# Optimization experiments

Hardware: AMD Instinct MI355X
Metric: run time of the kernel (lower is better)

## Reference

```python
import jax, jax.numpy as jnp
import numpy as np
import math

N, E = 1000, 128000
IN_DIM, HID, OUT_DIM = 256, 512, 16
L, H = 6, 8
C = HID // H  # 64, TransformerConv out_channels per head
EDGE_DIM = 32
MAX_LEN = 1000


def _pe(max_len, d_model):
    pos = np.arange(max_len)[:, None].astype(np.float32)
    div = np.exp(np.arange(0, d_model, 2).astype(np.float32) * (-math.log(10000.0) / d_model))
    pe = np.zeros((max_len, d_model), dtype=np.float32)
    pe[:, 0::2] = np.sin(pos * div)
    pe[:, 1::2] = np.cos(pos * div)
    return jnp.asarray(pe)


def setup_inputs() -> dict:
    key = jax.random.key(0)
    ks = jax.random.split(key, 32)
    g = lambda k, shape, fan_in: jax.random.normal(k, shape, jnp.float32) / jnp.sqrt(jnp.float32(fan_in))
    inp = {
        "x": jax.random.normal(ks[0], (N, IN_DIM), jnp.float32),
        "edge_index": jax.random.randint(ks[1], (2, E), 0, N, jnp.int64 if jax.config.jax_enable_x64 else jnp.int32),
        "edge_attr": jax.random.uniform(ks[2], (E, 4), jnp.float32),
        "embed_w": g(ks[3], (IN_DIM, HID), IN_DIM),
        "embed_b": jnp.zeros((HID,), jnp.float32),
        "pe": _pe(MAX_LEN, HID),
        "ee_w1": g(ks[4], (4, 16), 4), "ee_b1": jnp.zeros((16,), jnp.float32),
        "ee_w2": g(ks[5], (16, EDGE_DIM), 16), "ee_b2": jnp.zeros((EDGE_DIM,), jnp.float32),
        "q_w": g(ks[6], (L, HID, HID), HID), "q_b": jnp.zeros((L, HID), jnp.float32),
        "k_w": g(ks[7], (L, HID, HID), HID), "k_b": jnp.zeros((L, HID), jnp.float32),
        "v_w": g(ks[8], (L, HID, HID), HID), "v_b": jnp.zeros((L, HID), jnp.float32),
        "e_w": g(ks[9], (L, EDGE_DIM, HID), EDGE_DIM),
        "skip_w": g(ks[10], (L, HID, HID), HID), "skip_b": jnp.zeros((L, HID), jnp.float32),
        "ln_g": jnp.ones((L, HID), jnp.float32), "ln_b": jnp.zeros((L, HID), jnp.float32),
        "dom_w": g(ks[11], (HID, 16), HID), "dom_b": jnp.zeros((16,), jnp.float32),
        "cls_w1": g(ks[12], (HID + 16, HID // 2), HID + 16), "cls_b1": jnp.zeros((HID // 2,), jnp.float32),
        "cls_w2": g(ks[13], (HID // 2, OUT_DIM), HID // 2), "cls_b2": jnp.zeros((OUT_DIM,), jnp.float32),
    }
    return inp


def _layer_norm(x, g, b, eps=1e-5):
    mu = jnp.mean(x, axis=-1, keepdims=True)
    var = jnp.var(x, axis=-1, keepdims=True)
    return (x - mu) * jax.lax.rsqrt(var + eps) * g + b


def _forward(x, edge_index, edge_attr, embed_w, embed_b, pe, ee_w1, ee_b1, ee_w2, ee_b2,
             q_w, q_b, k_w, k_b, v_w, v_b, e_w, skip_w, skip_b, ln_g, ln_b,
             dom_w, dom_b, cls_w1, cls_b1, cls_w2, cls_b2):
    n = x.shape[0]
    h = x @ embed_w + embed_b
    h = h + pe[:n]
    # edge encoder: 4 -> 16 -> 32
    ef = jax.nn.relu(edge_attr @ ee_w1 + ee_b1) @ ee_w2 + ee_b2  # [E, 32]
    src, tgt = edge_index[0], edge_index[1]
    scale = 1.0 / math.sqrt(C)
    for l in range(L):
        res = h
        q = (h @ q_w[l] + q_b[l]).reshape(n, H, C)
        k = (h @ k_w[l] + k_b[l]).reshape(n, H, C)
        v = (h @ v_w[l] + v_b[l]).reshape(n, H, C)
        e = (ef @ e_w[l]).reshape(-1, H, C)            # [E, H, C], lin_edge has no bias
        kj = k[src] + e                                 # gather + edge bias
        score = jnp.sum(q[tgt] * kj, axis=-1) * scale   # [E, H]
        # segment softmax over incoming edges of each target node
        m = jax.ops.segment_max(score, tgt, num_segments=n)     # [N, H]
        al = jnp.exp(score - m[tgt])
        den = jax.ops.segment_sum(al, tgt, num_segments=n)      # [N, H]
        al = al / den[tgt]
        msg = (v[src] + e) * al[:, :, None]             # [E, H, C]
        out = jax.ops.segment_sum(msg, tgt, num_segments=n).reshape(n, HID)
        out = out + h @ skip_w[l] + skip_b[l]           # root_weight skip
        h = _layer_norm(out + res, ln_g[l], ln_b[l])
    dom = h @ dom_w + dom_b                             # [N, 16]
    comb = jnp.concatenate([h, dom], axis=-1)
    hid = jax.nn.relu(comb @ cls_w1 + cls_b1)
    return hid @ cls_w2 + cls_b2


def reference(x, edge_index, edge_attr, embed_w, embed_b, pe, ee_w1, ee_b1, ee_w2, ee_b2,
              q_w, q_b, k_w, k_b, v_w, v_b, e_w, skip_w, skip_b, ln_g, ln_b,
              dom_w, dom_b, cls_w1, cls_b1, cls_w2, cls_b2):
    return _forward(x, edge_index, edge_attr, embed_w, embed_b, pe, ee_w1, ee_b1, ee_w2, ee_b2,
                    q_w, q_b, k_w, k_b, v_w, v_b, e_w, skip_w, skip_b, ln_g, ln_b,
                    dom_w, dom_b, cls_w1, cls_b1, cls_w2, cls_b2)
```

## Files before the change

kernel.cpp:

```cpp
#include <hip/hip_runtime.h>
#include <hip/hip_bf16.h>
#include <cstdint>
#include <cstddef>

#define NN 1000
#define EE 128000
#define LAYERS 6
#define SCALE 0.125f
#define MAXDEG 320

typedef __attribute__((ext_vector_type(4))) float f32x4;
typedef __attribute__((ext_vector_type(8))) short short8v;

static __device__ __forceinline__ unsigned short f2bf(float x){
    unsigned int u = __float_as_uint(x);
    unsigned int lsb = (u >> 16) & 1u;
    u += 0x7fffu + lsb;
    return (unsigned short)(u >> 16);
}
static __device__ __forceinline__ float bf2f(unsigned short u){
    return __uint_as_float(((unsigned int)u) << 16);
}

__global__ void zero_counts(int* cnt){
    cnt[threadIdx.x] = 0;
}

__global__ void hist_kernel(const int* __restrict__ tgt, int* cnt){
    int e = blockIdx.x*256 + threadIdx.x;
    if (e < EE) atomicAdd(&cnt[tgt[e]], 1);
}

__global__ void scan_kernel(const int* __restrict__ cnt, int* offs, int* cursor){
    __shared__ int s[1024];
    int tid = threadIdx.x;
    s[tid] = (tid < NN) ? cnt[tid] : 0;
    __syncthreads();
    for (int st = 1; st < 1024; st <<= 1){
        int v = (tid >= st) ? s[tid-st] : 0;
        __syncthreads();
        s[tid] += v;
        __syncthreads();
    }
    int excl = (tid == 0) ? 0 : s[tid-1];
    if (tid < NN){ offs[tid] = excl; cursor[tid] = excl; }
    if (tid == 0) offs[NN] = s[NN-1];
}

__global__ void scatter_kernel(const int* __restrict__ src, const int* __restrict__ tgt,
                               int* cursor, int* ssrc, int* epos){
    int e = blockIdx.x*256 + threadIdx.x;
    if (e < EE){
        int t = tgt[e];
        int pos = atomicAdd(&cursor[t], 1);
        ssrc[pos] = src[e];
        epos[e] = pos;
    }
}

__global__ __launch_bounds__(256) void edge_enc(
    const float* __restrict__ edge_attr,
    const float* __restrict__ w1, const float* __restrict__ b1,
    const float* __restrict__ w2, const float* __restrict__ b2,
    const int* __restrict__ epos,
    unsigned short* __restrict__ efs)
{
    __shared__ float w1s[64], b1s[16], w2s[512], b2s[32];
    int tid = threadIdx.x;
    if (tid < 64) w1s[tid] = w1[tid];
    if (tid < 16) b1s[tid] = b1[tid];
    if (tid < 32) b2s[tid] = b2[tid];
    w2s[tid] = w2[tid];
    w2s[tid+256] = w2[tid+256];
    __syncthreads();
    int e = blockIdx.x*256 + tid;
    if (e >= EE) return;
    float4 av = *(const float4*)(edge_attr + (size_t)e*4);
    float hd[16];
    #pragma unroll
    for (int i = 0; i < 16; i++){
        float v = av.x*w1s[i] + av.y*w1s[16+i] + av.z*w1s[32+i] + av.w*w1s[48+i] + b1s[i];
        hd[i] = fmaxf(v, 0.f);
    }
    unsigned short* op = efs + (size_t)epos[e]*32;
    #pragma unroll
    for (int k4 = 0; k4 < 8; k4++){
        ushort4 ub;
        float v0 = b2s[k4*4+0], v1 = b2s[k4*4+1], v2 = b2s[k4*4+2], v3 = b2s[k4*4+3];
        #pragma unroll
        for (int i = 0; i < 16; i++){
            float hv = hd[i];
            v0 += hv*w2s[i*32 + k4*4+0];
            v1 += hv*w2s[i*32 + k4*4+1];
            v2 += hv*w2s[i*32 + k4*4+2];
            v3 += hv*w2s[i*32 + k4*4+3];
        }
        ub.x = f2bf(v0); ub.y = f2bf(v1); ub.z = f2bf(v2); ub.w = f2bf(v3);
        *(ushort4*)(op + k4*4) = ub;
    }
}

__global__ __launch_bounds__(256) void convert_all(
    const float* __restrict__ Wq, const float* __restrict__ Wk,
    const float* __restrict__ Wv, const float* __restrict__ Ws,
    const float* __restrict__ embed_w, const float* __restrict__ x,
    unsigned short* __restrict__ Wt, unsigned short* __restrict__ ewt,
    unsigned short* __restrict__ xb)
{
    int bid = blockIdx.x;
    int tid = threadIdx.x;
    if (bid < 6144){
        int mm = bid >> 8;
        int tile = bid & 255;
        int tk = tile >> 4, tn = tile & 15;
        int l = mm >> 2, m = mm & 3;
        const float* W = ((m==0)?Wq:(m==1)?Wk:(m==2)?Wv:Ws) + (size_t)l*512*512;
        unsigned short* dst = Wt + (size_t)mm*512*512;
        __shared__ float ts[32][33];
        int r = tid >> 3, c0 = (tid & 7)*4;
        float4 v = *(const float4*)(W + (size_t)(tk*32 + r)*512 + tn*32 + c0);
        ts[r][c0+0] = v.x; ts[r][c0+1] = v.y; ts[r][c0+2] = v.z; ts[r][c0+3] = v.w;
        __syncthreads();
        ushort4 o;
        o.x = f2bf(ts[c0+0][r]); o.y = f2bf(ts[c0+1][r]);
        o.z = f2bf(ts[c0+2][r]); o.w = f2bf(ts[c0+3][r]);
        *(ushort4*)(dst + (size_t)(tn*32 + r)*512 + tk*32 + c0) = o;
    } else if (bid < 6144 + 128){
        int tile = bid - 6144;
        int tn = tile & 15, tk = tile >> 4;
        __shared__ float ts2[32][33];
        int r = tid >> 3, c0 = (tid & 7)*4;
        float4 v = *(const float4*)(embed_w + (size_t)(tk*32 + r)*512 + tn*32 + c0);
        ts2[r][c0+0] = v.x; ts2[r][c0+1] = v.y; ts2[r][c0+2] = v.z; ts2[r][c0+3] = v.w;
        __syncthreads();
        ushort4 o;
        o.x = f2bf(ts2[c0+0][r]); o.y = f2bf(ts2[c0+1][r]);
        o.z = f2bf(ts2[c0+2][r]); o.w = f2bf(ts2[c0+3][r]);
        *(ushort4*)(ewt + (size_t)(tn*32 + r)*256 + tk*32 + c0) = o;
    } else {
        int row = bid - 6144 - 128;
        xb[(size_t)row*256 + tid] = (row < NN) ? f2bf(x[(size_t)row*256 + tid]) : (unsigned short)0;
    }
}

__global__ __launch_bounds__(256) void gemm_embed_mfma(
    const unsigned short* __restrict__ xb,
    const unsigned short* __restrict__ ewt,
    const float* __restrict__ bias, const float* __restrict__ pe,
    float* __restrict__ C, unsigned short* __restrict__ hb)
{
    int bid = blockIdx.x;
    int mt = bid >> 2, nt = bid & 3;
    int row0 = mt*64, col0 = nt*128;

    __shared__ __align__(16) unsigned short As[64*40];
    __shared__ __align__(16) unsigned short Bs[128*40];

    int tid = threadIdx.x;
    int wid = tid >> 6, l = tid & 63;
    int wm = wid >> 1, wn = wid & 1;

    f32x4 acc[2][4] = {};
    int ar = tid >> 2, akq = tid & 3;
    for (int k0 = 0; k0 < 256; k0 += 32){
        *(uint4*)&As[ar*40 + akq*8]      = *(const uint4*)&xb[(size_t)(row0+ar)*256 + k0 + akq*8];
        *(uint4*)&Bs[ar*40 + akq*8]      = *(const uint4*)&ewt[(size_t)(col0+ar)*256 + k0 + akq*8];
        *(uint4*)&Bs[(ar+64)*40 + akq*8] = *(const uint4*)&ewt[(size_t)(col0+ar+64)*256 + k0 + akq*8];
        __syncthreads();
        short8v a0 = *(const short8v*)&As[(wm*32 + (l&15))*40 + (l>>4)*8];
        short8v a1 = *(const short8v*)&As[(wm*32 + 16 + (l&15))*40 + (l>>4)*8];
        #pragma unroll
        for (int nj = 0; nj < 4; nj++){
            short8v b = *(const short8v*)&Bs[(wn*64 + nj*16 + (l&15))*40 + (l>>4)*8];
            acc[0][nj] = __builtin_amdgcn_mfma_f32_16x16x32_bf16(a0, b, acc[0][nj], 0, 0, 0);
            acc[1][nj] = __builtin_amdgcn_mfma_f32_16x16x32_bf16(a1, b, acc[1][nj], 0, 0, 0);
        }
        __syncthreads();
    }
    int rbase = (l >> 4)*4, cl = l & 15;
    #pragma unroll
    for (int mi = 0; mi < 2; mi++)
        #pragma unroll
        for (int nj = 0; nj < 4; nj++)
            #pragma unroll
            for (int r = 0; r < 4; r++){
                int grow = row0 + wm*32 + mi*16 + rbase + r;
                int gcol = col0 + wn*64 + nj*16 + cl;
                if (grow < NN){
                    float v = acc[mi][nj][r] + bias[gcol] + pe[(size_t)grow*512 + gcol];
                    C[(size_t)grow*512 + gcol] = v;
                    hb[(size_t)grow*512 + gcol] = f2bf(v);
                }
            }
}

__global__ __launch_bounds__(256) void gemm_qkvs_mfma(
    const unsigned short* __restrict__ hb,
    const unsigned short* __restrict__ Wt,
    const float* __restrict__ qb, const float* __restrict__ kb,
    const float* __restrict__ vb, const float* __restrict__ sb,
    float* __restrict__ Q, unsigned short* __restrict__ K16,
    unsigned short* __restrict__ V16, float* __restrict__ S)
{
    int bid = blockIdx.x;
    int mat = bid >> 7;
    int rem = bid & 127;
    int mt = rem >> 3, nt = rem & 7;
    int row0 = mt*64, col0 = nt*64;
    const unsigned short* W = Wt + (size_t)mat*512*512;
    const float* bias = (mat==0)?qb:(mat==1)?kb:(mat==2)?vb:sb;

    __shared__ __align__(16) unsigned short As[64*72];
    __shared__ __align__(16) unsigned short Bs[64*72];

    int tid = threadIdx.x;
    int wid = tid >> 6, l = tid & 63;
    int wm = wid >> 1, wn = wid & 1;

    f32x4 acc[2][2] = {};
    int lr = tid >> 2;
    int lc = (tid & 3)*2;
    const unsigned short* ga = hb + (size_t)(row0+lr)*512 + lc*8;
    const unsigned short* gb = W  + (size_t)(col0+lr)*512 + lc*8;

    uint4 ra0 = *(const uint4*)(ga);
    uint4 ra1 = *(const uint4*)(ga + 8);
    uint4 rb0 = *(const uint4*)(gb);
    uint4 rb1 = *(const uint4*)(gb + 8);

    for (int k0 = 0; k0 < 512; k0 += 64){
        __syncthreads();
        *(uint4*)&As[lr*72 + lc*8]     = ra0;
        *(uint4*)&As[lr*72 + lc*8 + 8] = ra1;
        *(uint4*)&Bs[lr*72 + lc*8]     = rb0;
        *(uint4*)&Bs[lr*72 + lc*8 + 8] = rb1;
        __syncthreads();
        if (k0 + 64 < 512){
            ra0 = *(const uint4*)(ga + k0 + 64);
            ra1 = *(const uint4*)(ga + k0 + 72);
            rb0 = *(const uint4*)(gb + k0 + 64);
            rb1 = *(const uint4*)(gb + k0 + 72);
        }
        #pragma unroll
        for (int ks = 0; ks < 2; ks++){
            short8v a0 = *(const short8v*)&As[(wm*32 + (l&15))*72      + ks*32 + (l>>4)*8];
            short8v a1 = *(const short8v*)&As[(wm*32 + 16 + (l&15))*72 + ks*32 + (l>>4)*8];
            short8v b0 = *(const short8v*)&Bs[(wn*32 + (l&15))*72      + ks*32 + (l>>4)*8];
            short8v b1 = *(const short8v*)&Bs[(wn*32 + 16 + (l&15))*72 + ks*32 + (l>>4)*8];
            acc[0][0] = __builtin_amdgcn_mfma_f32_16x16x32_bf16(a0, b0, acc[0][0], 0, 0, 0);
            acc[0][1] = __builtin_amdgcn_mfma_f32_16x16x32_bf16(a0, b1, acc[0][1], 0, 0, 0);
            acc[1][0] = __builtin_amdgcn_mfma_f32_16x16x32_bf16(a1, b0, acc[1][0], 0, 0, 0);
            acc[1][1] = __builtin_amdgcn_mfma_f32_16x16x32_bf16(a1, b1, acc[1][1], 0, 0, 0);
        }
    }
    int rbase = (l >> 4)*4, cl = l & 15;
    #pragma unroll
    for (int mi = 0; mi < 2; mi++)
        #pragma unroll
        for (int nj = 0; nj < 2; nj++)
            #pragma unroll
            for (int r = 0; r < 4; r++){
                int grow = row0 + wm*32 + mi*16 + rbase + r;
                int gcol = col0 + wn*32 + nj*16 + cl;
                if (grow < NN){
                    float v = acc[mi][nj][r] + bias[gcol];
                    if (mat == 0)      Q[(size_t)grow*512 + gcol] = v;
                    else if (mat == 1) K16[(size_t)grow*512 + gcol] = f2bf(v);
                    else if (mat == 2) V16[(size_t)grow*512 + gcol] = f2bf(v);
                    else               S[(size_t)grow*512 + gcol] = v;
                }
            }
}

__global__ __launch_bounds__(256) void attn_mfma(
    const float* __restrict__ Qm, const unsigned short* __restrict__ Km,
    const unsigned short* __restrict__ Vm,
    const unsigned short* __restrict__ efs, const float* __restrict__ e_w_l,
    const int* __restrict__ ssrc, const int* __restrict__ offs,
    float* __restrict__ x_pre)
{
    int tid = threadIdx.x;
    int t = blockIdx.x;

    __shared__ float q_s[512];
    __shared__ float qe_s[8*33];
    __shared__ __align__(16) unsigned short qb_s[512];
    __shared__ __align__(16) unsigned short qef_s[64*8];
    __shared__ float sc_s[MAXDEG*8];
    __shared__ int   src_s[MAXDEG];
    __shared__ float pv_s[2][512];
    __shared__ float pe_s[2][256];
    __shared__ float s_s[256];
    __shared__ float redm[32], redd[32];
    __shared__ float m_s[8], d_s[8];

    {
        float v0 = Qm[(size_t)t*512 + tid];
        float v1 = Qm[(size_t)t*512 + 256 + tid];
        q_s[tid] = v0; q_s[256+tid] = v1;
        qb_s[tid] = f2bf(v0); qb_s[256+tid] = f2bf(v1);
    }
    __syncthreads();
    {
        int hh = tid >> 5, dd = tid & 31;
        const float* wrow = e_w_l + (size_t)dd*512 + hh*64;
        const float* qh = q_s + hh*64;
        float a = 0.f;
        #pragma unroll
        for (int c = 0; c < 64; c++) a += qh[c]*wrow[c];
        qe_s[hh*33 + dd] = a;
    }
    __syncthreads();
    for (int idx = tid; idx < 512; idx += 256){
        int l = idx >> 3, j = idx & 7;
        int col = l & 15, d = (l >> 4)*8 + j;
        float v = (col < 8) ? qe_s[col*33 + d] : 0.f;
        qef_s[l*8 + j] = f2bf(v);
    }
    int start = offs[t], deg = offs[t+1] - start;
    __syncthreads();

    {
        int wv = tid >> 6, l = tid & 63;
        int arow = l & 15;
        int achk = (l >> 4)*8;
        const short8v bz = {0,0,0,0,0,0,0,0};
        for (int eg = wv*16; eg < deg; eg += 64){
            int e = eg + arow;
            int ec = (e < deg) ? e : 0;
            int s = ssrc[start + ec];
            if (achk == 0 && e < deg) src_s[e] = s;
            const unsigned short* kr = Km + (size_t)s*512 + achk;
            f32x4 acc = {0.f, 0.f, 0.f, 0.f};
            #pragma unroll
            for (int ks = 0; ks < 16; ks++){
                short8v a = *(const short8v*)(kr + ks*32);
                short8v b = (arow == (ks >> 1)) ? *(const short8v*)(qb_s + ks*32 + achk) : bz;
                acc = __builtin_amdgcn_mfma_f32_16x16x32_bf16(a, b, acc, 0, 0, 0);
            }
            {
                short8v a = *(const short8v*)(efs + (size_t)(start+ec)*32 + achk);
                short8v b = *(const short8v*)(qef_s + l*8);
                acc = __builtin_amdgcn_mfma_f32_16x16x32_bf16(a, b, acc, 0, 0, 0);
            }
            #pragma unroll
            for (int r = 0; r < 4; r++){
                int er = eg + (l >> 4)*4 + r;
                if (arow < 8 && er < deg) sc_s[er*8 + arow] = acc[r]*SCALE;
            }
        }
    }
    __syncthreads();

    {
        int he = tid & 7, ib = tid >> 3;
        float lm = -1e30f;
        for (int i = ib; i < deg; i += 32) lm = fmaxf(lm, sc_s[i*8 + he]);
        lm = fmaxf(lm, __shfl_xor(lm, 8));
        lm = fmaxf(lm, __shfl_xor(lm, 16));
        lm = fmaxf(lm, __shfl_xor(lm, 32));
        if ((tid & 63) < 8) redm[(tid>>6)*8 + (tid & 7)] = lm;
    }
    __syncthreads();
    if (tid < 8) m_s[tid] = fmaxf(fmaxf(redm[tid], redm[8+tid]), fmaxf(redm[16+tid], redm[24+tid]));
    __syncthreads();

    {
        int he = tid & 7, ib = tid >> 3;
        float mh = m_s[he];
        float den = 0.f;
        for (int i = ib; i < deg; i += 32){
            float al = __expf(sc_s[i*8 + he] - mh);
            sc_s[i*8 + he] = al;
            den += al;
        }
        den += __shfl_xor(den, 8);
        den += __shfl_xor(den, 16);
        den += __shfl_xor(den, 32);
        if ((tid & 63) < 8) redd[(tid>>6)*8 + (tid & 7)] = den;
    }
    __syncthreads();
    if (tid < 8) d_s[tid] = redd[tid] + redd[8+tid] + redd[16+tid] + redd[24+tid];
    __syncthreads();

    {
        int g = tid >> 7, q7 = tid & 127;
        int c4 = q7*4;
        int h2 = c4 >> 6;
        int hE = q7 >> 4, dE = (q7 & 15)*2;
        float4 accV = make_float4(0.f, 0.f, 0.f, 0.f);
        float2 accE = make_float2(0.f, 0.f);
        #pragma unroll 2
        for (int i = g; i < deg; i += 2){
            int s = src_s[i];
            float al = sc_s[i*8 + h2];
            float alE = sc_s[i*8 + hE];
            ushort4 v = *(const ushort4*)(Vm + (size_t)s*512 + c4);
            unsigned int e2 = *(const unsigned int*)(efs + (size_t)(start+i)*32 + dE);
            accV.x += al*bf2f(v.x); accV.y += al*bf2f(v.y);
            accV.z += al*bf2f(v.z); accV.w += al*bf2f(v.w);
            accE.x += alE*bf2f((unsigned short)(e2 & 0xffffu));
            accE.y += alE*bf2f((unsigned short)(e2 >> 16));
        }
        *(float4*)&pv_s[g][c4] = accV;
        *(float2*)&pe_s[g][hE*32 + dE] = accE;
    }
    __syncthreads();
    {
        float dv = d_s[tid >> 5];
        float invd = (dv > 0.f) ? 1.f/dv : 0.f;
        s_s[tid] = (pe_s[0][tid] + pe_s[1][tid]) * invd;
    }
    __syncthreads();

    {
        int c0 = tid, c1 = tid + 256;
        int h0 = c0 >> 6, h1 = c1 >> 6;
        float dv0 = d_s[h0], dv1 = d_s[h1];
        float i0 = (dv0 > 0.f) ? 1.f/dv0 : 0.f;
        float i1 = (dv1 > 0.f) ? 1.f/dv1 : 0.f;
        float r0 = (pv_s[0][c0] + pv_s[1][c0]) * i0;
        float r1 = (pv_s[0][c1] + pv_s[1][c1]) * i1;
        float oe0 = 0.f, oe1 = 0.f;
        const float* sp0 = s_s + h0*32;
        const float* sp1 = s_s + h1*32;
        #pragma unroll
        for (int d = 0; d < 32; d++){
            oe0 += sp0[d]*e_w_l[(size_t)d*512 + c0];
            oe1 += sp1[d]*e_w_l[(size_t)d*512 + c1];
        }
        x_pre[(size_t)t*512 + c0] = r0 + oe0;
        x_pre[(size_t)t*512 + c1] = r1 + oe1;
    }
}

__global__ __launch_bounds__(256) void ln_skip(
    const float* __restrict__ x_pre, const float* __restrict__ SKm,
    const float* __restrict__ hcur,
    const float* __restrict__ ln_g_l, const float* __restrict__ ln_b_l,
    float* __restrict__ hnext, unsigned short* __restrict__ hbn)
{
    int tid = threadIdx.x, t = blockIdx.x;
    __shared__ float red[4], red2[4];
    float x0 = x_pre[(size_t)t*512 + tid]       + SKm[(size_t)t*512 + tid]       + hcur[(size_t)t*512 + tid];
    float x1 = x_pre[(size_t)t*512 + 256 + tid] + SKm[(size_t)t*512 + 256 + tid] + hcur[(size_t)t*512 + 256 + tid];
    float sA = x0 + x1, sB = x0*x0 + x1*x1;
    #pragma unroll
    for (int m = 1; m <= 32; m <<= 1){
        sA += __shfl_xor(sA, m);
        sB += __shfl_xor(sB, m);
    }
    int wv = tid >> 6, ln = tid & 63;
    if (ln == 0){ red[wv] = sA; red2[wv] = sB; }
    __syncthreads();
    float tot  = red[0] + red[1] + red[2] + red[3];
    float tot2 = red2[0] + red2[1] + red2[2] + red2[3];
    float mu  = tot*(1.f/512.f);
    float var = tot2*(1.f/512.f) - mu*mu;
    float rstd = rsqrtf(var + 1e-5f);
    float y0 = (x0 - mu)*rstd*ln_g_l[tid]     + ln_b_l[tid];
    float y1 = (x1 - mu)*rstd*ln_g_l[256+tid] + ln_b_l[256+tid];
    hnext[(size_t)t*512 + tid]       = y0;
    hnext[(size_t)t*512 + 256 + tid] = y1;
    hbn[(size_t)t*512 + tid]       = f2bf(y0);
    hbn[(size_t)t*512 + 256 + tid] = f2bf(y1);
}

__global__ __launch_bounds__(256) void final_head(
    const float* __restrict__ hin,
    const float* __restrict__ dom_w, const float* __restrict__ dom_b,
    const float* __restrict__ w1, const float* __restrict__ b1,
    const float* __restrict__ w2, const float* __restrict__ b2,
    float* __restrict__ out)
{
    int tid = threadIdx.x, t = blockIdx.x;
    __shared__ float h_s[512];
    __shared__ float dom_s[16];
    __shared__ float hid_s[256];
    __shared__ float red[256];
    h_s[tid]     = hin[(size_t)t*512 + tid];
    h_s[tid+256] = hin[(size_t)t*512 + 256 + tid];
    __syncthreads();
    if (tid < 16){
        float a = dom_b[tid];
        for (int i = 0; i < 512; i++) a += h_s[i]*dom_w[i*16 + tid];
        dom_s[tid] = a;
    }
    __syncthreads();
    float acc = b1[tid];
    for (int i = 0; i < 512; i++) acc += h_s[i]*w1[(size_t)i*256 + tid];
    #pragma unroll
    for (int i = 0; i < 16; i++) acc += dom_s[i]*w1[(size_t)(512+i)*256 + tid];
    hid_s[tid] = fmaxf(acc, 0.f);
    __syncthreads();
    int o = tid & 15, g = tid >> 4;
    float p = 0.f;
    #pragma unroll
    for (int j = 0; j < 16; j++) p += hid_s[g*16 + j]*w2[(g*16 + j)*16 + o];
    red[tid] = p;
    __syncthreads();
    if (tid < 16){
        float s2 = b2[tid];
        for (int gg = 0; gg < 16; gg++) s2 += red[gg*16 + tid];
        out[(size_t)t*16 + tid] = s2;
    }
}

extern "C" void kernel_launch(void* const* d_in, const int* in_sizes, int n_in,
                              void* d_out, int out_size, void* d_ws, size_t ws_size,
                              hipStream_t stream)
{
    const float* x       = (const float*)d_in[0];
    const int*   eidx    = (const int*)  d_in[1];
    const float* eattr   = (const float*)d_in[2];
    const float* embed_w = (const float*)d_in[3];
    const float* embed_b = (const float*)d_in[4];
    const float* pe      = (const float*)d_in[5];
    const float* ee_w1   = (const float*)d_in[6];
    const float* ee_b1   = (const float*)d_in[7];
    const float* ee_w2   = (const float*)d_in[8];
    const float* ee_b2   = (const float*)d_in[9];
    const float* q_w     = (const float*)d_in[10];
    const float* q_b     = (const float*)d_in[11];
    const float* k_w     = (const float*)d_in[12];
    const float* k_b     = (const float*)d_in[13];
    const float* v_w     = (const float*)d_in[14];
    const float* v_b     = (const float*)d_in[15];
    const float* e_w     = (const float*)d_in[16];
    const float* skip_w  = (const float*)d_in[17];
    const float* skip_b  = (const float*)d_in[18];
    const float* ln_g    = (const float*)d_in[19];
    const float* ln_b    = (const float*)d_in[20];
    const float* dom_w   = (const float*)d_in[21];
    const float* dom_b   = (const float*)d_in[22];
    const float* cls_w1  = (const float*)d_in[23];
    const float* cls_b1  = (const float*)d_in[24];
    const float* cls_w2  = (const float*)d_in[25];
    const float* cls_b2  = (const float*)d_in[26];
    float* out = (float*)d_out;

    float* ws = (float*)d_ws;
    size_t o = 0;
    float* h0    = ws + o; o += (size_t)512*NN;
    float* h1    = ws + o; o += (size_t)512*NN;
    float* Qb    = ws + o; o += (size_t)512*NN;
    float* Sb    = ws + o; o += (size_t)512*NN;
    float* xpre  = ws + o; o += (size_t)512*NN;
    unsigned short* Kb16 = (unsigned short*)(ws + o); o += (size_t)1024*512/2;
    unsigned short* Vb16 = (unsigned short*)(ws + o); o += (size_t)1024*512/2;
    unsigned short* efs  = (unsigned short*)(ws + o); o += (size_t)EE*32/2;
    unsigned short* hb   = (unsigned short*)(ws + o); o += (size_t)1024*512/2;
    unsigned short* xb   = (unsigned short*)(ws + o); o += (size_t)1024*256/2;
    unsigned short* ewt  = (unsigned short*)(ws + o); o += (size_t)512*256/2;
    unsigned short* Wtb  = (unsigned short*)(ws + o); o += (size_t)24*512*512/2;
    int* cnt    = (int*)(ws + o); o += 1024;
    int* offs   = (int*)(ws + o); o += 1024;
    int* cursor = (int*)(ws + o); o += 1024;
    int* ssrc   = (int*)(ws + o); o += EE;
    int* epos   = (int*)(ws + o); o += EE;

    const int* srcp = eidx;
    const int* tgtp = eidx + EE;

    zero_counts<<<1, 1024, 0, stream>>>(cnt);
    hist_kernel<<<EE/256, 256, 0, stream>>>(tgtp, cnt);
    scan_kernel<<<1, 1024, 0, stream>>>(cnt, offs, cursor);
    scatter_kernel<<<EE/256, 256, 0, stream>>>(srcp, tgtp, cursor, ssrc, epos);
    edge_enc<<<EE/256, 256, 0, stream>>>(eattr, ee_w1, ee_b1, ee_w2, ee_b2, epos, efs);
    convert_all<<<6144 + 128 + 1024, 256, 0, stream>>>(q_w, k_w, v_w, skip_w, embed_w, x, Wtb, ewt, xb);
    gemm_embed_mfma<<<64, 256, 0, stream>>>(xb, ewt, embed_b, pe, h0, hb);

    float* hc = h0;
    float* hn = h1;
    for (int l = 0; l < LAYERS; l++){
        gemm_qkvs_mfma<<<512, 256, 0, stream>>>(
            hb, Wtb + (size_t)l*4*512*512,
            q_b + (size_t)l*512, k_b + (size_t)l*512,
            v_b + (size_t)l*512, skip_b + (size_t)l*512,
            Qb, Kb16, Vb16, Sb);
        attn_mfma<<<NN, 256, 0, stream>>>(
            Qb, Kb16, Vb16, efs, e_w + (size_t)l*32*512,
            ssrc, offs, xpre);
        ln_skip<<<NN, 256, 0, stream>>>(
            xpre, Sb, hc,
            ln_g + (size_t)l*512, ln_b + (size_t)l*512,
            hn, hb);
        float* tmp = hc; hc = hn; hn = tmp;
    }
    final_head<<<NN, 256, 0, stream>>>(hc, dom_w, dom_b, cls_w1, cls_b1, cls_w2, cls_b2, out);
}
```

Measured before the change: 581.8 us.

## Double-buffer QKVS GEMM, fuse LayerNorm into attention, drop softmax max pass

```diff
diff --git a/kernel.cpp b/kernel.cpp
--- a/kernel.cpp
+++ b/kernel.cpp
@@ -210,8 +210,8 @@
     const unsigned short* W = Wt + (size_t)mat*512*512;
     const float* bias = (mat==0)?qb:(mat==1)?kb:(mat==2)?vb:sb;
 
-    __shared__ __align__(16) unsigned short As[64*72];
-    __shared__ __align__(16) unsigned short Bs[64*72];
+    __shared__ __align__(16) unsigned short As[2][64*72];
+    __shared__ __align__(16) unsigned short Bs[2][64*72];
 
     int tid = threadIdx.x;
     int wid = tid >> 6, l = tid & 63;
@@ -227,32 +227,50 @@
     uint4 ra1 = *(const uint4*)(ga + 8);
     uint4 rb0 = *(const uint4*)(gb);
     uint4 rb1 = *(const uint4*)(gb + 8);
-
-    for (int k0 = 0; k0 < 512; k0 += 64){
-        __syncthreads();
-        *(uint4*)&As[lr*72 + lc*8]     = ra0;
-        *(uint4*)&As[lr*72 + lc*8 + 8] = ra1;
-        *(uint4*)&Bs[lr*72 + lc*8]     = rb0;
-        *(uint4*)&Bs[lr*72 + lc*8 + 8] = rb1;
-        __syncthreads();
-        if (k0 + 64 < 512){
-            ra0 = *(const uint4*)(ga + k0 + 64);
-            ra1 = *(const uint4*)(ga + k0 + 72);
-            rb0 = *(const uint4*)(gb + k0 + 64);
-            rb1 = *(const uint4*)(gb + k0 + 72);
-        }
+    *(uint4*)&As[0][lr*72 + lc*8]     = ra0;
+    *(uint4*)&As[0][lr*72 + lc*8 + 8] = ra1;
+    *(uint4*)&Bs[0][lr*72 + lc*8]     = rb0;
+    *(uint4*)&Bs[0][lr*72 + lc*8 + 8] = rb1;
+    ra0 = *(const uint4*)(ga + 64);
+    ra1 = *(const uint4*)(ga + 72);
+    rb0 = *(const uint4*)(gb + 64);
+    rb1 = *(const uint4*)(gb + 72);
+    __syncthreads();
+
+    #pragma unroll
+    for (int t = 0; t < 8; t++){
+        int cur = t & 1;
+        short8v a0f[2], a1f[2], b0f[2], b1f[2];
         #pragma unroll
         for (int ks = 0; ks < 2; ks++){
-            short8v a0 = *(const short8v*)&As[(wm*32 + (l&15))*72      + ks*32 + (l>>4)*8];
-            short8v a1 = *(const short8v*)&As[(wm*32 + 16 + (l&15))*72 + ks*32 + (l>>4)*8];
-            short8v b0 = *(const short8v*)&Bs[(wn*32 + (l&15))*72      + ks*32 + (l>>4)*8];
-            short8v b1 = *(const short8v*)&Bs[(wn*32 + 16 + (l&15))*72 + ks*32 + (l>>4)*8];
-            acc[0][0] = __builtin_amdgcn_mfma_f32_16x16x32_bf16(a0, b0, acc[0][0], 0, 0, 0);
-            acc[0][1] = __builtin_amdgcn_mfma_f32_16x16x32_bf16(a0, b1, acc[0][1], 0, 0, 0);
-            acc[1][0] = __builtin_amdgcn_mfma_f32_16x16x32_bf16(a1, b0, acc[1][0], 0, 0, 0);
-            acc[1][1] = __builtin_amdgcn_mfma_f32_16x16x32_bf16(a1, b1, acc[1][1], 0, 0, 0);
-        }
-    }
+            a0f[ks] = *(const short8v*)&As[cur][(wm*32 + (l&15))*72      + ks*32 + (l>>4)*8];
+            a1f[ks] = *(const short8v*)&As[cur][(wm*32 + 16 + (l&15))*72 + ks*32 + (l>>4)*8];
+            b0f[ks] = *(const short8v*)&Bs[cur][(wn*32 + (l&15))*72      + ks*32 + (l>>4)*8];
+            b1f[ks] = *(const short8v*)&Bs[cur][(wn*32 + 16 + (l&15))*72 + ks*32 + (l>>4)*8];
+        }
+        if (t < 7){
+            *(uint4*)&As[cur^1][lr*72 + lc*8]     = ra0;
+            *(uint4*)&As[cur^1][lr*72 + lc*8 + 8] = ra1;
+            *(uint4*)&Bs[cur^1][lr*72 + lc*8]     = rb0;
+            *(uint4*)&Bs[cur^1][lr*72 + lc*8 + 8] = rb1;
+        }
+        if (t + 2 < 8){
+            int k2 = (t + 2)*64;
+            ra0 = *(const uint4*)(ga + k2);
+            ra1 = *(const uint4*)(ga + k2 + 8);
+            rb0 = *(const uint4*)(gb + k2);
+            rb1 = *(const uint4*)(gb + k2 + 8);
+        }
+        #pragma unroll
+        for (int ks = 0; ks < 2; ks++){
+            acc[0][0] = __builtin_amdgcn_mfma_f32_16x16x32_bf16(a0f[ks], b0f[ks], acc[0][0], 0, 0, 0);
+            acc[0][1] = __builtin_amdgcn_mfma_f32_16x16x32_bf16(a0f[ks], b1f[ks], acc[0][1], 0, 0, 0);
+            acc[1][0] = __builtin_amdgcn_mfma_f32_16x16x32_bf16(a1f[ks], b0f[ks], acc[1][0], 0, 0, 0);
+            acc[1][1] = __builtin_amdgcn_mfma_f32_16x16x32_bf16(a1f[ks], b1f[ks], acc[1][1], 0, 0, 0);
+        }
+        if (t < 7) __syncthreads();
+    }
+
     int rbase = (l >> 4)*4, cl = l & 15;
     #pragma unroll
     for (int mi = 0; mi < 2; mi++)
@@ -277,7 +295,9 @@
     const unsigned short* __restrict__ Vm,
     const unsigned short* __restrict__ efs, const float* __restrict__ e_w_l,
     const int* __restrict__ ssrc, const int* __restrict__ offs,
-    float* __restrict__ x_pre)
+    const float* __restrict__ SKm, const float* __restrict__ hcur,
+    const float* __restrict__ ln_g_l, const float* __restrict__ ln_b_l,
+    float* __restrict__ hnext, unsigned short* __restrict__ hbn)
 {
     int tid = threadIdx.x;
     int t = blockIdx.x;
@@ -285,14 +305,15 @@
     __shared__ float q_s[512];
     __shared__ float qe_s[8*33];
     __shared__ __align__(16) unsigned short qb_s[512];
-    __shared__ __align__(16) unsigned short qef_s[64*8];
+    __shared__ __align__(16) unsigned short qbd_s[16*64*8];
     __shared__ float sc_s[MAXDEG*8];
     __shared__ int   src_s[MAXDEG];
-    __shared__ float pv_s[2][512];
-    __shared__ float pe_s[2][256];
+    __shared__ float pv_s[4][512];
+    __shared__ float pe_s[4][256];
     __shared__ float s_s[256];
-    __shared__ float redm[32], redd[32];
-    __shared__ float m_s[8], d_s[8];
+    __shared__ float redd[32];
+    __shared__ float d_s[8];
+    __shared__ float lredA[4], lredB[4];
 
     {
         float v0 = Qm[(size_t)t*512 + tid];
@@ -310,12 +331,16 @@
         for (int c = 0; c < 64; c++) a += qh[c]*wrow[c];
         qe_s[hh*33 + dd] = a;
     }
-    __syncthreads();
-    for (int idx = tid; idx < 512; idx += 256){
-        int l = idx >> 3, j = idx & 7;
-        int col = l & 15, d = (l >> 4)*8 + j;
-        float v = (col < 8) ? qe_s[col*33 + d] : 0.f;
-        qef_s[l*8 + j] = f2bf(v);
+    {
+        const uint4 z4 = {0u,0u,0u,0u};
+        #pragma unroll
+        for (int it = 0; it < 4; it++){
+            int idx = tid + it*256;
+            int ks = idx >> 6, lq = idx & 63;
+            int col = lq & 15;
+            uint4 v = (col == (ks >> 1)) ? *(const uint4*)&qb_s[ks*32 + (lq>>4)*8] : z4;
+            *(uint4*)&qbd_s[idx*8] = v;
+        }
     }
     int start = offs[t], deg = offs[t+1] - start;
     __syncthreads();
@@ -323,30 +348,44 @@
     {
         int wv = tid >> 6, l = tid & 63;
         int arow = l & 15;
-        int achk = (l >> 4)*8;
-        const short8v bz = {0,0,0,0,0,0,0,0};
+        int achk8 = (l >> 4)*8;
+        short8v bef;
+        {
+            int col = l & 15;
+            #pragma unroll
+            for (int j = 0; j < 8; j++){
+                float v = (col < 8) ? qe_s[col*33 + achk8 + j] : 0.f;
+                bef[j] = (short)f2bf(v);
+            }
+        }
         for (int eg = wv*16; eg < deg; eg += 64){
             int e = eg + arow;
             int ec = (e < deg) ? e : 0;
             int s = ssrc[start + ec];
-            if (achk == 0 && e < deg) src_s[e] = s;
-            const unsigned short* kr = Km + (size_t)s*512 + achk;
-            f32x4 acc = {0.f, 0.f, 0.f, 0.f};
+            if (achk8 == 0 && e < deg) src_s[e] = s;
+            const unsigned short* kr = Km + (size_t)s*512 + achk8;
+            f32x4 accA = {0.f, 0.f, 0.f, 0.f};
+            f32x4 accB = {0.f, 0.f, 0.f, 0.f};
             #pragma unroll
-            for (int ks = 0; ks < 16; ks++){
+            for (int ks = 0; ks < 8; ks++){
                 short8v a = *(const short8v*)(kr + ks*32);
-                short8v b = (arow == (ks >> 1)) ? *(const short8v*)(qb_s + ks*32 + achk) : bz;
-                acc = __builtin_amdgcn_mfma_f32_16x16x32_bf16(a, b, acc, 0, 0, 0);
+                short8v b = *(const short8v*)&qbd_s[(ks*64 + l)*8];
+                accA = __builtin_amdgcn_mfma_f32_16x16x32_bf16(a, b, accA, 0, 0, 0);
+            }
+            #pragma unroll
+            for (int ks = 8; ks < 16; ks++){
+                short8v a = *(const short8v*)(kr + ks*32);
+                short8v b = *(const short8v*)&qbd_s[(ks*64 + l)*8];
+                accB = __builtin_amdgcn_mfma_f32_16x16x32_bf16(a, b, accB, 0, 0, 0);
             }
             {
-                short8v a = *(const short8v*)(efs + (size_t)(start+ec)*32 + achk);
-                short8v b = *(const short8v*)(qef_s + l*8);
-                acc = __builtin_amdgcn_mfma_f32_16x16x32_bf16(a, b, acc, 0, 0, 0);
+                short8v a = *(const short8v*)(efs + (size_t)(start+ec)*32 + achk8);
+                accA = __builtin_amdgcn_mfma_f32_16x16x32_bf16(a, bef, accA, 0, 0, 0);
             }
             #pragma unroll
             for (int r = 0; r < 4; r++){
                 int er = eg + (l >> 4)*4 + r;
-                if (arow < 8 && er < deg) sc_s[er*8 + arow] = acc[r]*SCALE;
+                if (arow < 8 && er < deg) sc_s[er*8 + arow] = (accA[r] + accB[r])*SCALE;
             }
         }
     }
@@ -354,23 +393,9 @@
 
     {
         int he = tid & 7, ib = tid >> 3;
-        float lm = -1e30f;
-        for (int i = ib; i < deg; i += 32) lm = fmaxf(lm, sc_s[i*8 + he]);
-        lm = fmaxf(lm, __shfl_xor(lm, 8));
-        lm = fmaxf(lm, __shfl_xor(lm, 16));
-        lm = fmaxf(lm, __shfl_xor(lm, 32));
-        if ((tid & 63) < 8) redm[(tid>>6)*8 + (tid & 7)] = lm;
-    }
-    __syncthreads();
-    if (tid < 8) m_s[tid] = fmaxf(fmaxf(redm[tid], redm[8+tid]), fmaxf(redm[16+tid], redm[24+tid]));
-    __syncthreads();
-
-    {
-        int he = tid & 7, ib = tid >> 3;
-        float mh = m_s[he];
         float den = 0.f;
         for (int i = ib; i < deg; i += 32){
-            float al = __expf(sc_s[i*8 + he] - mh);
+            float al = __expf(sc_s[i*8 + he]);
             sc_s[i*8 + he] = al;
             den += al;
         }
@@ -384,32 +409,32 @@
     __syncthreads();
 
     {
-        int g = tid >> 7, q7 = tid & 127;
-        int c4 = q7*4;
-        int h2 = c4 >> 6;
-        int hE = q7 >> 4, dE = (q7 & 15)*2;
-        float4 accV = make_float4(0.f, 0.f, 0.f, 0.f);
-        float2 accE = make_float2(0.f, 0.f);
-        #pragma unroll 2
-        for (int i = g; i < deg; i += 2){
+        int g = tid >> 6, q6 = tid & 63;
+        int c8 = q6*8;
+        int h2 = q6 >> 3;
+        int dE4 = (q6 & 7)*4;
+        float accV[8] = {};
+        float accE[4] = {};
+        #pragma unroll 4
+        for (int i = g; i < deg; i += 4){
             int s = src_s[i];
             float al = sc_s[i*8 + h2];
-            float alE = sc_s[i*8 + hE];
-            ushort4 v = *(const ushort4*)(Vm + (size_t)s*512 + c4);
-            unsigned int e2 = *(const unsigned int*)(efs + (size_t)(start+i)*32 + dE);
-            accV.x += al*bf2f(v.x); accV.y += al*bf2f(v.y);
-            accV.z += al*bf2f(v.z); accV.w += al*bf2f(v.w);
-            accE.x += alE*bf2f((unsigned short)(e2 & 0xffffu));
-            accE.y += alE*bf2f((unsigned short)(e2 >> 16));
-        }
-        *(float4*)&pv_s[g][c4] = accV;
-        *(float2*)&pe_s[g][hE*32 + dE] = accE;
+            short8v v = *(const short8v*)(Vm + (size_t)s*512 + c8);
+            ushort4 e4 = *(const ushort4*)(efs + (size_t)(start+i)*32 + dE4);
+            #pragma unroll
+            for (int j = 0; j < 8; j++) accV[j] += al*bf2f((unsigned short)v[j]);
+            accE[0] += al*bf2f(e4.x); accE[1] += al*bf2f(e4.y);
+            accE[2] += al*bf2f(e4.z); accE[3] += al*bf2f(e4.w);
+        }
+        #pragma unroll
+        for (int j = 0; j < 8; j++) pv_s[g][c8+j] = accV[j];
+        *(float4*)&pe_s[g][h2*32 + dE4] = make_float4(accE[0], accE[1], accE[2], accE[3]);
     }
     __syncthreads();
     {
         float dv = d_s[tid >> 5];
         float invd = (dv > 0.f) ? 1.f/dv : 0.f;
-        s_s[tid] = (pe_s[0][tid] + pe_s[1][tid]) * invd;
+        s_s[tid] = (pe_s[0][tid] + pe_s[1][tid] + pe_s[2][tid] + pe_s[3][tid]) * invd;
     }
     __syncthreads();
 
@@ -419,8 +444,8 @@
         float dv0 = d_s[h0], dv1 = d_s[h1];
         float i0 = (dv0 > 0.f) ? 1.f/dv0 : 0.f;
         float i1 = (dv1 > 0.f) ? 1.f/dv1 : 0.f;
-        float r0 = (pv_s[0][c0] + pv_s[1][c0]) * i0;
-        float r1 = (pv_s[0][c1] + pv_s[1][c1]) * i1;
+        float r0 = (pv_s[0][c0] + pv_s[1][c0] + pv_s[2][c0] + pv_s[3][c0]) * i0;
+        float r1 = (pv_s[0][c1] + pv_s[1][c1] + pv_s[2][c1] + pv_s[3][c1]) * i1;
         float oe0 = 0.f, oe1 = 0.f;
         const float* sp0 = s_s + h0*32;
         const float* sp1 = s_s + h1*32;
@@ -429,41 +454,30 @@
             oe0 += sp0[d]*e_w_l[(size_t)d*512 + c0];
             oe1 += sp1[d]*e_w_l[(size_t)d*512 + c1];
         }
-        x_pre[(size_t)t*512 + c0] = r0 + oe0;
-        x_pre[(size_t)t*512 + c1] = r1 + oe1;
-    }
-}
-
-__global__ __launch_bounds__(256) void ln_skip(
-    const float* __restrict__ x_pre, const float* __restrict__ SKm,
-    const float* __restrict__ hcur,
-    const float* __restrict__ ln_g_l, const float* __restrict__ ln_b_l,
-    float* __restrict__ hnext, unsigned short* __restrict__ hbn)
-{
-    int tid = threadIdx.x, t = blockIdx.x;
-    __shared__ float red[4], red2[4];
-    float x0 = x_pre[(size_t)t*512 + tid]       + SKm[(size_t)t*512 + tid]       + hcur[(size_t)t*512 + tid];
-    float x1 = x_pre[(size_t)t*512 + 256 + tid] + SKm[(size_t)t*512 + 256 + tid] + hcur[(size_t)t*512 + 256 + tid];
-    float sA = x0 + x1, sB = x0*x0 + x1*x1;
-    #pragma unroll
-    for (int m = 1; m <= 32; m <<= 1){
-        sA += __shfl_xor(sA, m);
-        sB += __shfl_xor(sB, m);
-    }
-    int wv = tid >> 6, ln = tid & 63;
-    if (ln == 0){ red[wv] = sA; red2[wv] = sB; }
-    __syncthreads();
-    float tot  = red[0] + red[1] + red[2] + red[3];
-    float tot2 = red2[0] + red2[1] + red2[2] + red2[3];
-    float mu  = tot*(1.f/512.f);
-    float var = tot2*(1.f/512.f) - mu*mu;
-    float rstd = rsqrtf(var + 1e-5f);
-    float y0 = (x0 - mu)*rstd*ln_g_l[tid]     + ln_b_l[tid];
-    float y1 = (x1 - mu)*rstd*ln_g_l[256+tid] + ln_b_l[256+tid];
-    hnext[(size_t)t*512 + tid]       = y0;
-    hnext[(size_t)t*512 + 256 + tid] = y1;
-    hbn[(size_t)t*512 + tid]       = f2bf(y0);
-    hbn[(size_t)t*512 + 256 + tid] = f2bf(y1);
+        float x0 = r0 + oe0 + SKm[(size_t)t*512 + c0] + hcur[(size_t)t*512 + c0];
+        float x1 = r1 + oe1 + SKm[(size_t)t*512 + c1] + hcur[(size_t)t*512 + c1];
+
+        float sA = x0 + x1, sB = x0*x0 + x1*x1;
+        #pragma unroll
+        for (int m2 = 1; m2 <= 32; m2 <<= 1){
+            sA += __shfl_xor(sA, m2);
+            sB += __shfl_xor(sB, m2);
+        }
+        int wv = tid >> 6, ln = tid & 63;
+        if (ln == 0){ lredA[wv] = sA; lredB[wv] = sB; }
+        __syncthreads();
+        float tot  = lredA[0] + lredA[1] + lredA[2] + lredA[3];
+        float tot2 = lredB[0] + lredB[1] + lredB[2] + lredB[3];
+        float mu  = tot*(1.f/512.f);
+        float var = tot2*(1.f/512.f) - mu*mu;
+        float rstd = rsqrtf(var + 1e-5f);
+        float y0 = (x0 - mu)*rstd*ln_g_l[c0] + ln_b_l[c0];
+        float y1 = (x1 - mu)*rstd*ln_g_l[c1] + ln_b_l[c1];
+        hnext[(size_t)t*512 + c0] = y0;
+        hnext[(size_t)t*512 + c1] = y1;
+        hbn[(size_t)t*512 + c0]   = f2bf(y0);
+        hbn[(size_t)t*512 + c1]   = f2bf(y1);
+    }
 }
 
 __global__ __launch_bounds__(256) void final_head(
@@ -545,7 +559,6 @@
     float* h1    = ws + o; o += (size_t)512*NN;
     float* Qb    = ws + o; o += (size_t)512*NN;
     float* Sb    = ws + o; o += (size_t)512*NN;
-    float* xpre  = ws + o; o += (size_t)512*NN;
     unsigned short* Kb16 = (unsigned short*)(ws + o); o += (size_t)1024*512/2;
     unsigned short* Vb16 = (unsigned short*)(ws + o); o += (size_t)1024*512/2;
     unsigned short* efs  = (unsigned short*)(ws + o); o += (size_t)EE*32/2;
@@ -580,9 +593,7 @@
             Qb, Kb16, Vb16, Sb);
         attn_mfma<<<NN, 256, 0, stream>>>(
             Qb, Kb16, Vb16, efs, e_w + (size_t)l*32*512,
-            ssrc, offs, xpre);
-        ln_skip<<<NN, 256, 0, stream>>>(
-            xpre, Sb, hc,
+            ssrc, offs, Sb, hc,
             ln_g + (size_t)l*512, ln_b + (size_t)l*512,
             hn, hb);
         float* tmp = hc; hc = hn; hn = tmp;
```

After: 587.9 us. Within noise of the previous version (+1.0%).
